# Performance work log

Hardware: AMD Instinct MI355X
Metric: run time of the kernel (lower is better)

## Reference

```python
import jax, jax.numpy as jnp
import numpy as np

NUM_HEADS = 8
D_MODEL = 256
DIM = D_MODEL // NUM_HEADS  # 32
EPS = 1e-6


def _proj(x, W, b):
    # Conv1d with kernel_size=1 == channel-mixing matmul over length axis
    return jnp.einsum('oi,bil->bol', W, x) + b[None, :, None]


def _linear_attention(q, k, v):
    # q,k,v: [B, dim, heads, L]
    q = jax.nn.elu(q) + 1.0
    k = jax.nn.elu(k) + 1.0
    L = v.shape[3]
    v = v / L
    # KV: [B, dim_v, dim_k, heads]
    KV = jnp.einsum('bdhm,bqhm->bqdh', k, v)
    # Z: [B, heads, L]
    Z = 1.0 / (jnp.einsum('bdhm,bdh->bhm', q, k.sum(3)) + EPS)
    # out: [B, dim, heads, L]
    return jnp.einsum('bdhm,bqdh,bhm->bqhm', q, KV, Z) * L


def setup_inputs() -> dict:
    key = jax.random.key(0)
    ks = jax.random.split(key, 11)
    B, L = 8, 4096
    s = 0.05
    return {
        'query': jax.random.normal(ks[0], (B, D_MODEL, L), dtype=jnp.float32),
        'key':   jax.random.normal(ks[1], (B, D_MODEL, L), dtype=jnp.float32),
        'value': jax.random.normal(ks[2], (B, D_MODEL, L), dtype=jnp.float32),
        'Wq': jax.random.normal(ks[3], (D_MODEL, D_MODEL), dtype=jnp.float32) * s,
        'bq': jnp.zeros((D_MODEL,), dtype=jnp.float32),
        'Wk': jax.random.normal(ks[4], (D_MODEL, D_MODEL), dtype=jnp.float32) * s,
        'bk': jnp.zeros((D_MODEL,), dtype=jnp.float32),
        'Wv': jax.random.normal(ks[5], (D_MODEL, D_MODEL), dtype=jnp.float32) * s,
        'bv': jnp.zeros((D_MODEL,), dtype=jnp.float32),
        'Wm': jax.random.normal(ks[6], (D_MODEL, D_MODEL), dtype=jnp.float32) * s,
        'bm': jnp.zeros((D_MODEL,), dtype=jnp.float32),
    }


def reference(query, key, value, Wq, bq, Wk, bk, Wv, bv, Wm, bm):
    B = query.shape[0]
    q = _proj(query, Wq, bq).reshape(B, DIM, NUM_HEADS, -1)
    k = _proj(key,   Wk, bk).reshape(B, DIM, NUM_HEADS, -1)
    v = _proj(value, Wv, bv).reshape(B, DIM, NUM_HEADS, -1)
    x = _linear_attention(q, k, v)           # [B, dim, heads, L]
    x = x.reshape(B, D_MODEL, -1)            # merge heads back to channels
    return jnp.einsum('oi,bil->bol', Wm, x) + bm[None, :, None]
```

## Files before the change

kernel.cpp:

```cpp
#include <hip/hip_runtime.h>
#include <math.h>

#define D_MODEL 256
#define NHEADS 8
#define HDIM 32
#define BATCH 8
#define SEQL 4096
#define EPS 1e-6f

typedef _Float16 f16;
typedef _Float16 f16x4 __attribute__((ext_vector_type(4)));
typedef _Float16 f16x8 __attribute__((ext_vector_type(8)));
typedef float f32x4 __attribute__((ext_vector_type(4)));

__device__ __forceinline__ float elu1(float x) {
    return x > 0.f ? x + 1.f : __expf(x);
}

__global__ void prep_kernel(const float* __restrict__ Wq, const float* __restrict__ Wk,
                            const float* __restrict__ Wv, const float* __restrict__ Wm,
                            const float* __restrict__ bq, const float* __restrict__ bk,
                            const float* __restrict__ bv,
                            f16* __restrict__ w16, float* __restrict__ bperm) {
    const int bid = blockIdx.x;
    if (bid < 1024) {
        int idx = bid * 256 + threadIdx.x;
        int mat = idx >> 16;
        int r = idx & 65535;
        int e = r & 7;
        int lane = (r >> 3) & 63;
        int kstep = (r >> 9) & 7;
        int ostrip = r >> 12;
        int o = ostrip * 16 + (lane & 15);
        int k = kstep * 32 + (lane >> 4) * 8 + e;
        const float* W = (mat == 0) ? Wq : (mat == 1) ? Wk : (mat == 2) ? Wv : Wm;
        float v;
        if (mat < 3) v = W[(size_t)(((o & 31) << 3) + (o >> 5)) * 256 + k];
        else         v = W[(size_t)o * 256 + (((k & 31) << 3) + (k >> 5))];
        w16[idx] = (f16)v;
    } else {
        int t = threadIdx.x;
        bperm[0 * 256 + t] = bq[((t & 31) << 3) + (t >> 5)];
        bperm[1 * 256 + t] = bk[((t & 31) << 3) + (t >> 5)];
        bperm[2 * 256 + t] = bv[((t & 31) << 3) + (t >> 5)];
    }
}

#define XSTR 264
__global__ __launch_bounds__(256, 3) void gemm_stage1(
    const float* __restrict__ Xq, const float* __restrict__ Xk, const float* __restrict__ Xv,
    const f16* __restrict__ w16, const float* __restrict__ bperm,
    f16* __restrict__ yq, f16* __restrict__ yk, f16* __restrict__ yv) {
    __shared__ __align__(16) f16 Xs[64 * XSTR];
    f16* Cb = Xs;

    const int z = blockIdx.z;
    const int which = z >> 3;
    const int b = z & 7;
    const float* X = (which == 0) ? Xq : (which == 1) ? Xk : Xv;
    const f16* W = w16 + which * 65536;
    f16* Y = (which == 0) ? yq : (which == 1) ? yk : yv;
    const float* bp = bperm + which * 256;

    const int l0 = blockIdx.x * 64;
    const int tid = threadIdx.x;
    const int wave = tid >> 6, lane = tid & 63;
    const int ln = lane & 15, quad = lane >> 4;
    const int kq = tid >> 4;
    const int lg = tid & 15;

    const float* Xbase = X + ((size_t)(b * D_MODEL) + 4 * kq) * SEQL + l0 + 4 * lg;

    float4 xa[4], xb[4];

#define LOADX(DST, C) do { \
        const float* xp_ = Xbase + (size_t)(64 * (C)) * SEQL; \
        DST[0] = *(const float4*)(xp_ + 0 * SEQL); \
        DST[1] = *(const float4*)(xp_ + 1 * SEQL); \
        DST[2] = *(const float4*)(xp_ + 2 * SEQL); \
        DST[3] = *(const float4*)(xp_ + 3 * SEQL); \
    } while (0)

#define STOREB(SRC, C) do { \
        f16x4 w_; \
        w_[0] = (f16)SRC[0].x; w_[1] = (f16)SRC[1].x; w_[2] = (f16)SRC[2].x; w_[3] = (f16)SRC[3].x; \
        *(f16x4*)&Xs[(4 * lg + 0) * XSTR + 64 * (C) + 4 * kq] = w_; \
        w_[0] = (f16)SRC[0].y; w_[1] = (f16)SRC[1].y; w_[2] = (f16)SRC[2].y; w_[3] = (f16)SRC[3].y; \
        *(f16x4*)&Xs[(4 * lg + 1) * XSTR + 64 * (C) + 4 * kq] = w_; \
        w_[0] = (f16)SRC[0].z; w_[1] = (f16)SRC[1].z; w_[2] = (f16)SRC[2].z; w_[3] = (f16)SRC[3].z; \
        *(f16x4*)&Xs[(4 * lg + 2) * XSTR + 64 * (C) + 4 * kq] = w_; \
        w_[0] = (f16)SRC[0].w; w_[1] = (f16)SRC[1].w; w_[2] = (f16)SRC[2].w; w_[3] = (f16)SRC[3].w; \
        *(f16x4*)&Xs[(4 * lg + 3) * XSTR + 64 * (C) + 4 * kq] = w_; \
    } while (0)

    f32x4 acc[4][4];
#pragma unroll
    for (int mf = 0; mf < 4; ++mf)
#pragma unroll
        for (int nf = 0; nf < 4; ++nf)
#pragma unroll
            for (int r = 0; r < 4; ++r) acc[mf][nf][r] = 0.f;

    LOADX(xa, 0);
    LOADX(xb, 1);
    STOREB(xa, 0);
    LOADX(xa, 2);
    STOREB(xb, 1);
    LOADX(xb, 3);
    STOREB(xa, 2);
    STOREB(xb, 3);
    __syncthreads();

    const f16* Wl = W + lane * 8;
    f16x8 afc[4], afn[4];
#pragma unroll
    for (int mf = 0; mf < 4; ++mf)
        afc[mf] = *(const f16x8*)(Wl + (wave * 32 + mf * 8 + 0) * 512);
#pragma unroll
    for (int s = 0; s < 8; ++s) {
        const int k0 = s * 32;
        if (s < 7) {
#pragma unroll
            for (int mf = 0; mf < 4; ++mf)
                afn[mf] = *(const f16x8*)(Wl + (wave * 32 + mf * 8 + s + 1) * 512);
        }
        f16x8 bf[4];
#pragma unroll
        for (int nf = 0; nf < 4; ++nf)
            bf[nf] = *(const f16x8*)&Xs[(nf * 16 + ln) * XSTR + k0 + quad * 8];
#pragma unroll
        for (int mf = 0; mf < 4; ++mf)
#pragma unroll
            for (int nf = 0; nf < 4; ++nf)
                acc[mf][nf] = __builtin_amdgcn_mfma_f32_16x16x32_f16(afc[mf], bf[nf], acc[mf][nf], 0, 0, 0);
#pragma unroll
        for (int mf = 0; mf < 4; ++mf) afc[mf] = afn[mf];
    }

    float bv_[4][4];
#pragma unroll
    for (int mf = 0; mf < 4; ++mf)
#pragma unroll
        for (int r = 0; r < 4; ++r)
            bv_[mf][r] = bp[wave * 64 + mf * 16 + quad * 4 + r];
    __syncthreads();
#pragma unroll
    for (int mf = 0; mf < 4; ++mf)
#pragma unroll
        for (int nf = 0; nf < 4; ++nf) {
            f16x4 w;
#pragma unroll
            for (int r = 0; r < 4; ++r) w[r] = (f16)(acc[mf][nf][r] + bv_[mf][r]);
            *(f16x4*)&Cb[(nf * 16 + ln) * XSTR + wave * 64 + mf * 16 + quad * 4] = w;
        }
    __syncthreads();
    {
        const int rw = tid >> 3, sg = tid & 7;
#pragma unroll
        for (int u = 0; u < 8; ++u) {
            const int row = (u & 1) * 32 + rw;
            const int col = (u >> 1) * 64 + sg * 8;
            *(f16x8*)(Y + ((size_t)(b * SEQL + l0 + row)) * 256 + col) =
                *(const f16x8*)&Cb[row * XSTR + col];
        }
    }
#undef LOADX
#undef STOREB
}

#define KVLP 66
#define NSPLIT 16
__global__ __launch_bounds__(256) void kv_mfma(
    const f16* __restrict__ kp, const f16* __restrict__ vp,
    float* __restrict__ KVpart, float* __restrict__ ksum_part) {
    __shared__ __align__(16) f16 kT[32 * KVLP];
    __shared__ __align__(16) f16 vT[48 * KVLP];
    const int ls = blockIdx.x;
    const int bh = blockIdx.y;
    const int b = bh >> 3, h = bh & 7;
    const int t = threadIdx.x;
    const int wave = t >> 6, lane = t & 63;
    const int ln = lane & 15, quad = lane >> 4;
    const int lrow = t >> 2, seg = t & 3;

    {
        const int rr = 32 + (t >> 4), c0 = (t & 15) * 4;
        f16x4 w;
        const f16 one = (f16)1.f, zero = (f16)0.f;
        w[0] = w[1] = w[2] = w[3] = (rr == 32) ? one : zero;
        *(f16x4*)&vT[rr * KVLP + c0] = w;
    }

    const int tiP = wave >> 1, tjP = wave & 1;
    f32x4 accP, accS;
#pragma unroll
    for (int r = 0; r < 4; ++r) { accP[r] = 0.f; accS[r] = 0.f; }

    for (int ch = 0; ch < 4; ++ch) {
        __syncthreads();
        const size_t goff = ((size_t)(b * SEQL + ls * 256 + ch * 64 + lrow)) * 256 + h * 32 + seg * 8;
        f16x8 k8 = *(const f16x8*)(kp + goff);
        f16x8 v8 = *(const f16x8*)(vp + goff);
#pragma unroll
        for (int j = 0; j < 8; ++j) {
            kT[(seg * 8 + j) * KVLP + lrow] = (f16)elu1((float)k8[j]);
            vT[(seg * 8 + j) * KVLP + lrow] = v8[j];
        }
        __syncthreads();
#pragma unroll
        for (int ks = 0; ks < 2; ++ks) {
            const int kc = ks * 32 + quad * 8;
            f16x8 bP = *(const f16x8*)&kT[(tjP * 16 + ln) * KVLP + kc];
            f16x8 aP = *(const f16x8*)&vT[(tiP * 16 + ln) * KVLP + kc];
            accP = __builtin_amdgcn_mfma_f32_16x16x32_f16(aP, bP, accP, 0, 0, 0);
            if (wave < 2) {
                f16x8 aS = *(const f16x8*)&vT[(32 + ln) * KVLP + kc];
                accS = __builtin_amdgcn_mfma_f32_16x16x32_f16(aS, bP, accS, 0, 0, 0);
            }
        }
    }

    float* KVp = KVpart + ((size_t)ls * 64 + bh) * 1024;
#pragma unroll
    for (int r = 0; r < 4; ++r)
        KVp[(tiP * 16 + quad * 4 + r) * 32 + tjP * 16 + ln] = accP[r];
    if (wave < 2 && quad == 0)
        ksum_part[((size_t)ls * 64 + bh) * 32 + tjP * 16 + ln] = accS[0];
}

__global__ __launch_bounds__(256) void kv_reduce(
    const float* __restrict__ KVpart, const float* __restrict__ ksum_part,
    float* __restrict__ KVfin, float* __restrict__ ksum_f) {
    const int bh = blockIdx.x;
    const int t = threadIdx.x;
    const float* src = KVpart + (size_t)bh * 1024 + t * 4;
    float ax = 0.f, ay = 0.f, az = 0.f, aw = 0.f;
#pragma unroll
    for (int s = 0; s < NSPLIT; ++s) {
        float4 p = *(const float4*)(src + (size_t)s * 65536);
        ax += p.x; ay += p.y; az += p.z; aw += p.w;
    }
    float4 o; o.x = ax; o.y = ay; o.z = az; o.w = aw;
    *(float4*)(KVfin + (size_t)bh * 1024 + t * 4) = o;
    if (t < 32) {
        float ss = 0.f;
#pragma unroll
        for (int s = 0; s < NSPLIT; ++s)
            ss += ksum_part[((size_t)s * 64 + bh) * 32 + t];
        ksum_f[bh * 32 + t] = ss;
    }
}

__global__ __launch_bounds__(256) void attn_out_kernel(
    const f16* __restrict__ qp, const float* __restrict__ KV,
    const float* __restrict__ ksum, const f16* __restrict__ wm16,
    const float* __restrict__ bm, float* __restrict__ out) {
    __shared__ __align__(16) f16 xs[64 * 264];
    __shared__ __align__(16) f16 Baug[8 * 48 * 40];
    __shared__ float dens[8][64];
    const int b = blockIdx.y;
    const int l0 = blockIdx.x * 64;
    const int t = threadIdx.x;
    const int wave = t >> 6, lane = t & 63;
    const int ln = lane & 15, quad = lane >> 4;

    {
        const int h = t >> 5, qd = t & 31;
        const float* kvp = KV + ((size_t)(b * NHEADS + h) * HDIM + qd) * HDIM;
        f16* dst = &Baug[(h * 48 + qd) * 40];
#pragma unroll
        for (int i = 0; i < 32; i += 4) {
            float4 a = *(const float4*)(kvp + i);
            f16x4 w4;
            w4[0] = (f16)a.x; w4[1] = (f16)a.y; w4[2] = (f16)a.z; w4[3] = (f16)a.w;
            *(f16x4*)(dst + i) = w4;
        }
        Baug[(h * 48 + 32) * 40 + qd] = (f16)ksum[(size_t)(b * NHEADS + h) * HDIM + qd];
    }
    {
        const int rbase = t >> 5, ch = (t & 31) * 8;
        const f16* qr = qp + ((size_t)(b * SEQL + l0 + rbase)) * 256 + ch;
        f16* dst = &xs[rbase * 264 + ch];
#pragma unroll
        for (int p = 0; p < 8; ++p) {
            f16x8 v = *(const f16x8*)(qr + (size_t)(p * 8) * 256);
            f16x8 w;
#pragma unroll
            for (int j = 0; j < 8; ++j) w[j] = (f16)elu1((float)v[j]);
            *(f16x8*)(dst + p * 8 * 264) = w;
        }
    }
    __syncthreads();
#pragma unroll
    for (int hh = 0; hh < 2; ++hh) {
        const int h = wave * 2 + hh;
        f16x8 a_s[4], b_s[3];
#pragma unroll
        for (int mf = 0; mf < 4; ++mf)
            a_s[mf] = *(const f16x8*)&xs[(mf * 16 + ln) * 264 + h * 32 + quad * 8];
#pragma unroll
        for (int nf = 0; nf < 3; ++nf)
            b_s[nf] = *(const f16x8*)&Baug[(h * 48 + nf * 16 + ln) * 40 + quad * 8];
        f32x4 C[4][3];
#pragma unroll
        for (int mf = 0; mf < 4; ++mf)
#pragma unroll
            for (int nf = 0; nf < 3; ++nf) {
#pragma unroll
                for (int r = 0; r < 4; ++r) C[mf][nf][r] = 0.f;
                C[mf][nf] = __builtin_amdgcn_mfma_f32_16x16x32_f16(a_s[mf], b_s[nf], C[mf][nf], 0, 0, 0);
            }
        if (ln == 0) {
#pragma unroll
            for (int mf = 0; mf < 4; ++mf)
#pragma unroll
                for (int r = 0; r < 4; ++r)
                    dens[h][mf * 16 + quad * 4 + r] = C[mf][2][r];
        }
        __syncthreads();
#pragma unroll
        for (int mf = 0; mf < 4; ++mf)
#pragma unroll
            for (int r = 0; r < 4; ++r) {
                const int l = mf * 16 + quad * 4 + r;
                const float rd = __builtin_amdgcn_rcpf(dens[h][l] + EPS);
#pragma unroll
                for (int nf = 0; nf < 2; ++nf)
                    xs[l * 264 + h * 32 + nf * 16 + ln] = (f16)(C[mf][nf][r] * rd);
            }
        __syncthreads();
    }
    f32x4 acc[4][4];
#pragma unroll
    for (int mf = 0; mf < 4; ++mf)
#pragma unroll
        for (int nf = 0; nf < 4; ++nf)
#pragma unroll
            for (int r = 0; r < 4; ++r) acc[mf][nf][r] = 0.f;
    const f16* Wl = wm16 + lane * 8;
    f16x8 afc[4], afn[4];
#pragma unroll
    for (int mf = 0; mf < 4; ++mf)
        afc[mf] = *(const f16x8*)(Wl + (wave * 32 + mf * 8 + 0) * 512);
#pragma unroll
    for (int it = 0; it < 8; ++it) {
        const int k0 = it * 32;
        if (it < 7) {
#pragma unroll
            for (int mf = 0; mf < 4; ++mf)
                afn[mf] = *(const f16x8*)(Wl + (wave * 32 + mf * 8 + it + 1) * 512);
        }
        f16x8 bf[4];
#pragma unroll
        for (int nf = 0; nf < 4; ++nf)
            bf[nf] = *(const f16x8*)&xs[(nf * 16 + ln) * 264 + k0 + quad * 8];
#pragma unroll
        for (int mf = 0; mf < 4; ++mf)
#pragma unroll
            for (int nf = 0; nf < 4; ++nf)
                acc[mf][nf] = __builtin_amdgcn_mfma_f32_16x16x32_f16(afc[mf], bf[nf], acc[mf][nf], 0, 0, 0);
#pragma unroll
        for (int mf = 0; mf < 4; ++mf) afc[mf] = afn[mf];
    }
    float* Of = (float*)xs;
    __syncthreads();
#pragma unroll
    for (int p = 0; p < 2; ++p) {
        if ((wave >> 1) == p) {
            const int rb = (wave & 1) * 64;
#pragma unroll
            for (int mf = 0; mf < 4; ++mf)
#pragma unroll
                for (int r = 0; r < 4; ++r) {
                    const int o = wave * 64 + mf * 16 + quad * 4 + r;
                    const float bb = bm[o];
                    const int row = rb + mf * 16 + quad * 4 + r;
#pragma unroll
                    for (int nf = 0; nf < 4; ++nf)
                        Of[row * 66 + nf * 16 + ln] = acc[mf][nf][r] + bb;
                }
        }
        __syncthreads();
        {
            const int rw = t >> 4, lc = (t & 15) * 4;
#pragma unroll
            for (int rnd = 0; rnd < 8; ++rnd) {
                const int row = rnd * 16 + rw;
                float4 v4 = *(const float4*)&Of[row * 66 + lc];
                *(float4*)(out + ((size_t)(b * D_MODEL + p * 128 + row)) * SEQL + l0 + lc) = v4;
            }
        }
        __syncthreads();
    }
}

extern "C" void kernel_launch(void* const* d_in, const int* in_sizes, int n_in,
                              void* d_out, int out_size, void* d_ws, size_t ws_size,
                              hipStream_t stream) {
    const float* query = (const float*)d_in[0];
    const float* key_  = (const float*)d_in[1];
    const float* value = (const float*)d_in[2];
    const float* Wq = (const float*)d_in[3];
    const float* bq = (const float*)d_in[4];
    const float* Wk = (const float*)d_in[5];
    const float* bk = (const float*)d_in[6];
    const float* Wv = (const float*)d_in[7];
    const float* bv = (const float*)d_in[8];
    const float* Wm = (const float*)d_in[9];
    const float* bm = (const float*)d_in[10];

    char* w = (char*)d_ws;
    f16*   w16    = (f16*)w;
    float* bperm  = (float*)(w + 524288);
    float* KVpart = (float*)(w + 528384);
    float* ksum_p = (float*)(w + 4722688);
    float* KVfin  = (float*)(w + 4853760);
    float* ksum_f = (float*)(w + 5115904);
    f16*   qp     = (f16*)(w + 5124096);
    f16*   kp     = qp + (size_t)BATCH * SEQL * 256;
    f16*   vp     = kp + (size_t)BATCH * SEQL * 256;

    prep_kernel<<<1025, 256, 0, stream>>>(Wq, Wk, Wv, Wm, bq, bk, bv, w16, bperm);

    gemm_stage1<<<dim3(SEQL / 64, 1, 24), 256, 0, stream>>>(
        query, key_, value, w16, bperm, qp, kp, vp);

    kv_mfma<<<dim3(NSPLIT, BATCH * NHEADS), 256, 0, stream>>>(kp, vp, KVpart, ksum_p);

    kv_reduce<<<dim3(BATCH * NHEADS), 256, 0, stream>>>(KVpart, ksum_p, KVfin, ksum_f);

    attn_out_kernel<<<dim3(SEQL / 64, BATCH), 256, 0, stream>>>(
        qp, KVfin, ksum_f, w16 + 3 * 65536, bm, (float*)d_out);
}
```

Baseline: 193.6 us.

## Process two sequence tiles per block with prefetch overlap and swizzled LDS

The stage-1 projection GEMM now handles 128 sequence positions per block in two 64-wide halves. The global loads for the second half are issued before the first half's MFMA compute, and the data is staged in a second LDS buffer. An XOR swizzle is added to the LDS X layout to reduce bank conflicts on the transposed stores and fragment reads. This raises LDS use and register pressure, lowers occupancy hint to 2 blocks/SIMD and halves the grid size.

```diff
diff --git a/kernel.cpp b/kernel.cpp
--- a/kernel.cpp
+++ b/kernel.cpp
@@ -47,12 +47,12 @@
 }
 
 #define XSTR 264
-__global__ __launch_bounds__(256, 3) void gemm_stage1(
+__global__ __launch_bounds__(256, 2) void gemm_stage1(
     const float* __restrict__ Xq, const float* __restrict__ Xk, const float* __restrict__ Xv,
     const f16* __restrict__ w16, const float* __restrict__ bperm,
     f16* __restrict__ yq, f16* __restrict__ yk, f16* __restrict__ yv) {
-    __shared__ __align__(16) f16 Xs[64 * XSTR];
-    f16* Cb = Xs;
+    __shared__ __align__(16) f16 B0[64 * XSTR];
+    __shared__ __align__(16) f16 B1[64 * XSTR];
 
     const int z = blockIdx.z;
     const int which = z >> 3;
@@ -62,110 +62,124 @@
     f16* Y = (which == 0) ? yq : (which == 1) ? yk : yv;
     const float* bp = bperm + which * 256;
 
-    const int l0 = blockIdx.x * 64;
+    const int l0 = blockIdx.x * 128;
     const int tid = threadIdx.x;
     const int wave = tid >> 6, lane = tid & 63;
     const int ln = lane & 15, quad = lane >> 4;
     const int kq = tid >> 4;
     const int lg = tid & 15;
+    const int swm = 8 * (lg & 3);
+    const int swr = 8 * ((ln >> 2) & 3);
 
     const float* Xbase = X + ((size_t)(b * D_MODEL) + 4 * kq) * SEQL + l0 + 4 * lg;
 
-    float4 xa[4], xb[4];
-
-#define LOADX(DST, C) do { \
-        const float* xp_ = Xbase + (size_t)(64 * (C)) * SEQL; \
+    float4 xa[4], xb[4], xc[4], xd[4];
+
+#define LOADX(DST, LOFF, C) do { \
+        const float* xp_ = Xbase + (LOFF) + (size_t)(64 * (C)) * SEQL; \
         DST[0] = *(const float4*)(xp_ + 0 * SEQL); \
         DST[1] = *(const float4*)(xp_ + 1 * SEQL); \
         DST[2] = *(const float4*)(xp_ + 2 * SEQL); \
         DST[3] = *(const float4*)(xp_ + 3 * SEQL); \
     } while (0)
 
-#define STOREB(SRC, C) do { \
+#define STOREB(SRC, BUF, C) do { \
+        const int c_ = ((64 * (C) + 4 * kq) ^ swm); \
         f16x4 w_; \
         w_[0] = (f16)SRC[0].x; w_[1] = (f16)SRC[1].x; w_[2] = (f16)SRC[2].x; w_[3] = (f16)SRC[3].x; \
-        *(f16x4*)&Xs[(4 * lg + 0) * XSTR + 64 * (C) + 4 * kq] = w_; \
+        *(f16x4*)&BUF[(4 * lg + 0) * XSTR + c_] = w_; \
         w_[0] = (f16)SRC[0].y; w_[1] = (f16)SRC[1].y; w_[2] = (f16)SRC[2].y; w_[3] = (f16)SRC[3].y; \
-        *(f16x4*)&Xs[(4 * lg + 1) * XSTR + 64 * (C) + 4 * kq] = w_; \
+        *(f16x4*)&BUF[(4 * lg + 1) * XSTR + c_] = w_; \
         w_[0] = (f16)SRC[0].z; w_[1] = (f16)SRC[1].z; w_[2] = (f16)SRC[2].z; w_[3] = (f16)SRC[3].z; \
-        *(f16x4*)&Xs[(4 * lg + 2) * XSTR + 64 * (C) + 4 * kq] = w_; \
+        *(f16x4*)&BUF[(4 * lg + 2) * XSTR + c_] = w_; \
         w_[0] = (f16)SRC[0].w; w_[1] = (f16)SRC[1].w; w_[2] = (f16)SRC[2].w; w_[3] = (f16)SRC[3].w; \
-        *(f16x4*)&Xs[(4 * lg + 3) * XSTR + 64 * (C) + 4 * kq] = w_; \
+        *(f16x4*)&BUF[(4 * lg + 3) * XSTR + c_] = w_; \
     } while (0)
 
     f32x4 acc[4][4];
-#pragma unroll
-    for (int mf = 0; mf < 4; ++mf)
-#pragma unroll
-        for (int nf = 0; nf < 4; ++nf)
-#pragma unroll
-            for (int r = 0; r < 4; ++r) acc[mf][nf][r] = 0.f;
-
-    LOADX(xa, 0);
-    LOADX(xb, 1);
-    STOREB(xa, 0);
-    LOADX(xa, 2);
-    STOREB(xb, 1);
-    LOADX(xb, 3);
-    STOREB(xa, 2);
-    STOREB(xb, 3);
+#define ZEROACC() do { \
+        _Pragma("unroll") for (int mf = 0; mf < 4; ++mf) \
+        _Pragma("unroll") for (int nf = 0; nf < 4; ++nf) \
+        _Pragma("unroll") for (int r = 0; r < 4; ++r) acc[mf][nf][r] = 0.f; \
+    } while (0)
+
+#define COMPUTE(BUF) do { \
+        const f16* Wl = W + lane * 8; \
+        f16x8 afc[4], afn[4]; \
+        _Pragma("unroll") for (int mf = 0; mf < 4; ++mf) \
+            afc[mf] = *(const f16x8*)(Wl + (wave * 32 + mf * 8 + 0) * 512); \
+        _Pragma("unroll") for (int s = 0; s < 8; ++s) { \
+            const int k0 = s * 32; \
+            if (s < 7) { \
+                _Pragma("unroll") for (int mf = 0; mf < 4; ++mf) \
+                    afn[mf] = *(const f16x8*)(Wl + (wave * 32 + mf * 8 + s + 1) * 512); \
+            } \
+            f16x8 bf[4]; \
+            _Pragma("unroll") for (int nf = 0; nf < 4; ++nf) \
+                bf[nf] = *(const f16x8*)&BUF[(nf * 16 + ln) * XSTR + ((k0 + quad * 8) ^ swr)]; \
+            _Pragma("unroll") for (int mf = 0; mf < 4; ++mf) \
+            _Pragma("unroll") for (int nf = 0; nf < 4; ++nf) \
+                acc[mf][nf] = __builtin_amdgcn_mfma_f32_16x16x32_f16(afc[mf], bf[nf], acc[mf][nf], 0, 0, 0); \
+            _Pragma("unroll") for (int mf = 0; mf < 4; ++mf) afc[mf] = afn[mf]; \
+        } \
+    } while (0)
+
+#define EPILOG(BUF, LX) do { \
+        float bv_[4][4]; \
+        _Pragma("unroll") for (int mf = 0; mf < 4; ++mf) \
+        _Pragma("unroll") for (int r = 0; r < 4; ++r) \
+            bv_[mf][r] = bp[wave * 64 + mf * 16 + quad * 4 + r]; \
+        _Pragma("unroll") for (int mf = 0; mf < 4; ++mf) \
+        _Pragma("unroll") for (int nf = 0; nf < 4; ++nf) { \
+            f16x4 w; \
+            _Pragma("unroll") for (int r = 0; r < 4; ++r) w[r] = (f16)(acc[mf][nf][r] + bv_[mf][r]); \
+            *(f16x4*)&BUF[(nf * 16 + ln) * XSTR + wave * 64 + mf * 16 + quad * 4] = w; \
+        } \
+        __syncthreads(); \
+        { \
+            const int rw = tid >> 3, sg = tid & 7; \
+            _Pragma("unroll") for (int u = 0; u < 8; ++u) { \
+                const int row = (u & 1) * 32 + rw; \
+                const int col = (u >> 1) * 64 + sg * 8; \
+                *(f16x8*)(Y + ((size_t)(b * SEQL + (LX) + row)) * 256 + col) = \
+                    *(const f16x8*)&BUF[row * XSTR + col]; \
+            } \
+        } \
+    } while (0)
+
+    LOADX(xa, 0, 0);
+    LOADX(xb, 0, 1);
+    STOREB(xa, B0, 0);
+    LOADX(xa, 0, 2);
+    STOREB(xb, B0, 1);
+    LOADX(xb, 0, 3);
+    STOREB(xa, B0, 2);
+    STOREB(xb, B0, 3);
     __syncthreads();
 
-    const f16* Wl = W + lane * 8;
-    f16x8 afc[4], afn[4];
-#pragma unroll
-    for (int mf = 0; mf < 4; ++mf)
-        afc[mf] = *(const f16x8*)(Wl + (wave * 32 + mf * 8 + 0) * 512);
-#pragma unroll
-    for (int s = 0; s < 8; ++s) {
-        const int k0 = s * 32;
-        if (s < 7) {
-#pragma unroll
-            for (int mf = 0; mf < 4; ++mf)
-                afn[mf] = *(const f16x8*)(Wl + (wave * 32 + mf * 8 + s + 1) * 512);
-        }
-        f16x8 bf[4];
-#pragma unroll
-        for (int nf = 0; nf < 4; ++nf)
-            bf[nf] = *(const f16x8*)&Xs[(nf * 16 + ln) * XSTR + k0 + quad * 8];
-#pragma unroll
-        for (int mf = 0; mf < 4; ++mf)
-#pragma unroll
-            for (int nf = 0; nf < 4; ++nf)
-                acc[mf][nf] = __builtin_amdgcn_mfma_f32_16x16x32_f16(afc[mf], bf[nf], acc[mf][nf], 0, 0, 0);
-#pragma unroll
-        for (int mf = 0; mf < 4; ++mf) afc[mf] = afn[mf];
-    }
-
-    float bv_[4][4];
-#pragma unroll
-    for (int mf = 0; mf < 4; ++mf)
-#pragma unroll
-        for (int r = 0; r < 4; ++r)
-            bv_[mf][r] = bp[wave * 64 + mf * 16 + quad * 4 + r];
+    LOADX(xa, 64, 0);
+    LOADX(xb, 64, 1);
+    LOADX(xc, 64, 2);
+    LOADX(xd, 64, 3);
+    ZEROACC();
+    COMPUTE(B0);
+    STOREB(xa, B1, 0);
+    STOREB(xb, B1, 1);
+    STOREB(xc, B1, 2);
+    STOREB(xd, B1, 3);
     __syncthreads();
-#pragma unroll
-    for (int mf = 0; mf < 4; ++mf)
-#pragma unroll
-        for (int nf = 0; nf < 4; ++nf) {
-            f16x4 w;
-#pragma unroll
-            for (int r = 0; r < 4; ++r) w[r] = (f16)(acc[mf][nf][r] + bv_[mf][r]);
-            *(f16x4*)&Cb[(nf * 16 + ln) * XSTR + wave * 64 + mf * 16 + quad * 4] = w;
-        }
+    EPILOG(B0, l0);
+
+    ZEROACC();
+    COMPUTE(B1);
     __syncthreads();
-    {
-        const int rw = tid >> 3, sg = tid & 7;
-#pragma unroll
-        for (int u = 0; u < 8; ++u) {
-            const int row = (u & 1) * 32 + rw;
-            const int col = (u >> 1) * 64 + sg * 8;
-            *(f16x8*)(Y + ((size_t)(b * SEQL + l0 + row)) * 256 + col) =
-                *(const f16x8*)&Cb[row * XSTR + col];
-        }
-    }
+    EPILOG(B1, l0 + 64);
+
 #undef LOADX
 #undef STOREB
+#undef ZEROACC
+#undef COMPUTE
+#undef EPILOG
 }
 
 #define KVLP 66
@@ -422,7 +436,7 @@
 
     prep_kernel<<<1025, 256, 0, stream>>>(Wq, Wk, Wv, Wm, bq, bk, bv, w16, bperm);
 
-    gemm_stage1<<<dim3(SEQL / 64, 1, 24), 256, 0, stream>>>(
+    gemm_stage1<<<dim3(SEQL / 128, 1, 24), 256, 0, stream>>>(
         query, key_, value, w16, bperm, qp, kp, vp);
 
     kv_mfma<<<dim3(NSPLIT, BATCH * NHEADS), 256, 0, stream>>>(kp, vp, KVpart, ksum_p);
```

After: 198.5 us. +2.5%, slower.

## Swizzle stage-1 LDS tile and precompute fragment-ordered f16 KV operand in reducer

Applied to the files above, without the earlier changes.

XOR-swizzles the shared-memory column index in the stage-1 projection GEMM so the transposed stores and MFMA B-fragment loads hit fewer bank conflicts. The KV reducer now writes KV and the key sum directly as f16 in MFMA lane-fragment order, zero-padding the augmented block. The output kernel then loads its B operands straight from global memory instead of every block converting and staging KV into LDS. This removes redundant per-block conversion work and LDS traffic, at the cost of a more intricate layout contract between kernels.

```diff
diff --git a/kernel.cpp b/kernel.cpp
--- a/kernel.cpp
+++ b/kernel.cpp
@@ -9,6 +9,7 @@
 #define EPS 1e-6f
 
 typedef _Float16 f16;
+typedef _Float16 f16x2 __attribute__((ext_vector_type(2)));
 typedef _Float16 f16x4 __attribute__((ext_vector_type(4)));
 typedef _Float16 f16x8 __attribute__((ext_vector_type(8)));
 typedef float f32x4 __attribute__((ext_vector_type(4)));
@@ -68,6 +69,8 @@
     const int ln = lane & 15, quad = lane >> 4;
     const int kq = tid >> 4;
     const int lg = tid & 15;
+    const int swm = 8 * (lg & 3);
+    const int swr = 8 * ((ln >> 2) & 3);
 
     const float* Xbase = X + ((size_t)(b * D_MODEL) + 4 * kq) * SEQL + l0 + 4 * lg;
 
@@ -82,15 +85,16 @@
     } while (0)
 
 #define STOREB(SRC, C) do { \
+        const int c_ = (64 * (C) + 4 * kq) ^ swm; \
         f16x4 w_; \
         w_[0] = (f16)SRC[0].x; w_[1] = (f16)SRC[1].x; w_[2] = (f16)SRC[2].x; w_[3] = (f16)SRC[3].x; \
-        *(f16x4*)&Xs[(4 * lg + 0) * XSTR + 64 * (C) + 4 * kq] = w_; \
+        *(f16x4*)&Xs[(4 * lg + 0) * XSTR + c_] = w_; \
         w_[0] = (f16)SRC[0].y; w_[1] = (f16)SRC[1].y; w_[2] = (f16)SRC[2].y; w_[3] = (f16)SRC[3].y; \
-        *(f16x4*)&Xs[(4 * lg + 1) * XSTR + 64 * (C) + 4 * kq] = w_; \
+        *(f16x4*)&Xs[(4 * lg + 1) * XSTR + c_] = w_; \
         w_[0] = (f16)SRC[0].z; w_[1] = (f16)SRC[1].z; w_[2] = (f16)SRC[2].z; w_[3] = (f16)SRC[3].z; \
-        *(f16x4*)&Xs[(4 * lg + 2) * XSTR + 64 * (C) + 4 * kq] = w_; \
+        *(f16x4*)&Xs[(4 * lg + 2) * XSTR + c_] = w_; \
         w_[0] = (f16)SRC[0].w; w_[1] = (f16)SRC[1].w; w_[2] = (f16)SRC[2].w; w_[3] = (f16)SRC[3].w; \
-        *(f16x4*)&Xs[(4 * lg + 3) * XSTR + 64 * (C) + 4 * kq] = w_; \
+        *(f16x4*)&Xs[(4 * lg + 3) * XSTR + c_] = w_; \
     } while (0)
 
     f32x4 acc[4][4];
@@ -127,7 +131,7 @@
         f16x8 bf[4];
 #pragma unroll
         for (int nf = 0; nf < 4; ++nf)
-            bf[nf] = *(const f16x8*)&Xs[(nf * 16 + ln) * XSTR + k0 + quad * 8];
+            bf[nf] = *(const f16x8*)&Xs[(nf * 16 + ln) * XSTR + ((k0 + quad * 8) ^ swr)];
 #pragma unroll
         for (int mf = 0; mf < 4; ++mf)
 #pragma unroll
@@ -230,7 +234,7 @@
 
 __global__ __launch_bounds__(256) void kv_reduce(
     const float* __restrict__ KVpart, const float* __restrict__ ksum_part,
-    float* __restrict__ KVfin, float* __restrict__ ksum_f) {
+    f16* __restrict__ KVaug) {
     const int bh = blockIdx.x;
     const int t = threadIdx.x;
     const float* src = KVpart + (size_t)bh * 1024 + t * 4;
@@ -240,23 +244,36 @@
         float4 p = *(const float4*)(src + (size_t)s * 65536);
         ax += p.x; ay += p.y; az += p.z; aw += p.w;
     }
-    float4 o; o.x = ax; o.y = ay; o.z = az; o.w = aw;
-    *(float4*)(KVfin + (size_t)bh * 1024 + t * 4) = o;
+    {
+        const int qd = t >> 3, c = t & 7;
+        const int nf = qd >> 4, lnq = qd & 15, quad = c >> 1;
+        const int lane = quad * 16 + lnq;
+        f16x4 w4;
+        w4[0] = (f16)ax; w4[1] = (f16)ay; w4[2] = (f16)az; w4[3] = (f16)aw;
+        *(f16x4*)&KVaug[((size_t)(bh * 3) + nf) * 512 + lane * 8 + (c & 1) * 4] = w4;
+    }
+    f16* aug2 = KVaug + ((size_t)(bh * 3) + 2) * 512;
     if (t < 32) {
         float ss = 0.f;
 #pragma unroll
         for (int s = 0; s < NSPLIT; ++s)
             ss += ksum_part[((size_t)s * 64 + bh) * 32 + t];
-        ksum_f[bh * 32 + t] = ss;
+        aug2[(size_t)((t >> 3) * 16) * 8 + (t & 7)] = (f16)ss;
+    }
+    {
+        const int lane2 = t >> 2;
+        if ((lane2 & 15) != 0) {
+            f16x2 z; z[0] = (f16)0.f; z[1] = (f16)0.f;
+            *(f16x2*)&aug2[t * 2] = z;
+        }
     }
 }
 
 __global__ __launch_bounds__(256) void attn_out_kernel(
-    const f16* __restrict__ qp, const float* __restrict__ KV,
-    const float* __restrict__ ksum, const f16* __restrict__ wm16,
-    const float* __restrict__ bm, float* __restrict__ out) {
+    const f16* __restrict__ qp, const f16* __restrict__ KVaug,
+    const f16* __restrict__ wm16, const float* __restrict__ bm,
+    float* __restrict__ out) {
     __shared__ __align__(16) f16 xs[64 * 264];
-    __shared__ __align__(16) f16 Baug[8 * 48 * 40];
     __shared__ float dens[8][64];
     const int b = blockIdx.y;
     const int l0 = blockIdx.x * 64;
@@ -265,19 +282,6 @@
     const int ln = lane & 15, quad = lane >> 4;
 
     {
-        const int h = t >> 5, qd = t & 31;
-        const float* kvp = KV + ((size_t)(b * NHEADS + h) * HDIM + qd) * HDIM;
-        f16* dst = &Baug[(h * 48 + qd) * 40];
-#pragma unroll
-        for (int i = 0; i < 32; i += 4) {
-            float4 a = *(const float4*)(kvp + i);
-            f16x4 w4;
-            w4[0] = (f16)a.x; w4[1] = (f16)a.y; w4[2] = (f16)a.z; w4[3] = (f16)a.w;
-            *(f16x4*)(dst + i) = w4;
-        }
-        Baug[(h * 48 + 32) * 40 + qd] = (f16)ksum[(size_t)(b * NHEADS + h) * HDIM + qd];
-    }
-    {
         const int rbase = t >> 5, ch = (t & 31) * 8;
         const f16* qr = qp + ((size_t)(b * SEQL + l0 + rbase)) * 256 + ch;
         f16* dst = &xs[rbase * 264 + ch];
@@ -294,13 +298,14 @@
 #pragma unroll
     for (int hh = 0; hh < 2; ++hh) {
         const int h = wave * 2 + hh;
+        const f16* kvb = KVaug + ((size_t)((b * NHEADS + h) * 3)) * 512 + lane * 8;
         f16x8 a_s[4], b_s[3];
+#pragma unroll
+        for (int nf = 0; nf < 3; ++nf)
+            b_s[nf] = *(const f16x8*)(kvb + nf * 512);
 #pragma unroll
         for (int mf = 0; mf < 4; ++mf)
             a_s[mf] = *(const f16x8*)&xs[(mf * 16 + ln) * 264 + h * 32 + quad * 8];
-#pragma unroll
-        for (int nf = 0; nf < 3; ++nf)
-            b_s[nf] = *(const f16x8*)&Baug[(h * 48 + nf * 16 + ln) * 40 + quad * 8];
         f32x4 C[4][3];
 #pragma unroll
         for (int mf = 0; mf < 4; ++mf)
@@ -414,9 +419,8 @@
     float* bperm  = (float*)(w + 524288);
     float* KVpart = (float*)(w + 528384);
     float* ksum_p = (float*)(w + 4722688);
-    float* KVfin  = (float*)(w + 4853760);
-    float* ksum_f = (float*)(w + 5115904);
-    f16*   qp     = (f16*)(w + 5124096);
+    f16*   KVaug  = (f16*)(w + 4853760);
+    f16*   qp     = (f16*)(w + 5050368);
     f16*   kp     = qp + (size_t)BATCH * SEQL * 256;
     f16*   vp     = kp + (size_t)BATCH * SEQL * 256;
 
@@ -427,8 +431,8 @@
 
     kv_mfma<<<dim3(NSPLIT, BATCH * NHEADS), 256, 0, stream>>>(kp, vp, KVpart, ksum_p);
 
-    kv_reduce<<<dim3(BATCH * NHEADS), 256, 0, stream>>>(KVpart, ksum_p, KVfin, ksum_f);
+    kv_reduce<<<dim3(BATCH * NHEADS), 256, 0, stream>>>(KVpart, ksum_p, KVaug);
 
     attn_out_kernel<<<dim3(SEQL / 64, BATCH), 256, 0, stream>>>(
-        qp, KVfin, ksum_f, w16 + 3 * 65536, bm, (float*)d_out);
-}
+        qp, KVaug, w16 + 3 * 65536, bm, (float*)d_out);
+}
```

New measurement: 195.2 us. About the same (+0.8%).
